# Performance work log

Hardware: AMD Instinct MI355X
Metric: run time of the kernel (lower is better)

The kernel has to match this reference:

```python
import jax, jax.numpy as jnp
import numpy as np
import math

B, H, S, D = 2, 12, 2048, 64

def setup_inputs() -> dict:
    key = jax.random.key(0)
    kq, kk, kv, km = jax.random.split(key, 4)
    Q = jax.random.normal(kq, (B, H, S, D), dtype=jnp.float32)
    K = jax.random.normal(kk, (B, H, S, D), dtype=jnp.float32)
    V = jax.random.normal(kv, (B, H, S, D), dtype=jnp.float32)
    mask = jax.random.randint(km, (B, 1, S, S), 0, 2, dtype=jnp.int32)
    return {"Q": Q, "K": K, "V": V, "mask": mask}

def reference(Q, K, V, mask):
    d_k = K.shape[-1]
    # [B,H,S,S] scores
    scores = jnp.einsum('bhqd,bhkd->bhqk', Q, K) / math.sqrt(d_k)
    scores = jnp.where(mask == 0, jnp.float32(-1e20), scores)
    attn = jax.nn.softmax(scores, axis=-1)
    # dropout p=0 -> identity
    return jnp.einsum('bhqk,bhkd->bhqd', attn, V)
```

## Files before the change

### kernel.cpp

```cpp
#include <hip/hip_runtime.h>
#include <hip/hip_bf16.h>
#include <math.h>


#define BB 2
#define HH 12
#define SS 2048
#define DD 64
#define BQ 128
#define BK 64
#define GG 2
#define KG (SS / GG)
#define NTG (KG / BK)
#define NQB (SS / BQ)
#define NBH (BB * HH)
#define LT 76
#define NROWS (BB * HH * SS)
#define QSCALE 0.1803368801111f

typedef __attribute__((ext_vector_type(8))) short bf8_t;
typedef __attribute__((ext_vector_type(4))) short bf4_t;
typedef __attribute__((ext_vector_type(4))) float f4_t;
typedef __attribute__((ext_vector_type(4))) unsigned u4_t;
typedef unsigned long long u64;

__device__ __forceinline__ short f2bf(float f) {
    __hip_bfloat16 h = __float2bfloat16(f);
    return *reinterpret_cast<short*>(&h);
}

__device__ __forceinline__ void gl_lds16(const void* g, void* l) {
    __builtin_amdgcn_global_load_lds(
        (const __attribute__((address_space(1))) unsigned*)(g),
        (__attribute__((address_space(3))) unsigned*)(l), 16, 0, 0);
}

__device__ __forceinline__ bf8_t ldfrag(const unsigned short* buf, int row, int c8) {
    return *(const bf8_t*)&buf[((row << 3) | (c8 ^ (row & 7))) << 3];
}

__global__ __launch_bounds__(256) void prepass(
    const float* __restrict__ V, const float* __restrict__ K,
    const int* __restrict__ M, unsigned short* __restrict__ Vt,
    unsigned short* __restrict__ Kb, u64* __restrict__ Mbt)
{
    __shared__ unsigned short Ts[64][LT];
    const int bx   = blockIdx.x;
    const int tid  = threadIdx.x;
    const int w    = tid >> 6;
    const int lane = tid & 63;
    const int b    = bx >> 11;
    const int row  = bx & 2047;

    {
        const int* src = M + (size_t)bx * SS;
        #pragma unroll
        for (int p = 0; p < 8; ++p) {
            int k = p * 256 + w * 64 + lane;
            u64 bm = __ballot(src[k] != 0);
            if (lane == 0)
                Mbt[(size_t)b * 32 * SS + (size_t)(p * 4 + w) * SS + row] = bm;
        }
    }

    if (bx < 768) {
        const int s0 = (bx & 31) * 64;
        const int bh = bx >> 5;
        const float* Vg = V + (size_t)bh * SS * DD;
        #pragma unroll
        for (int pass = 0; pass < 4; ++pass) {
            int c = tid + pass * 256;
            int r = c >> 4, col = (c & 15) * 4;
            float4 v = *(const float4*)(Vg + (size_t)(s0 + r) * DD + col);
            bf4_t p; p.x = f2bf(v.x); p.y = f2bf(v.y); p.z = f2bf(v.z); p.w = f2bf(v.w);
            *(bf4_t*)&Ts[r][col] = p;
        }
        __syncthreads();
        unsigned short* Vo = Vt + (size_t)bh * DD * SS;
        #pragma unroll
        for (int pass = 0; pass < 2; ++pass) {
            int c = tid + pass * 256;
            int d = c >> 3, sc = (c & 7) * 8;
            const int hh32 = sc & 32;
            const int qq4  = (sc >> 1) & 12;
            unsigned short t[8];
            #pragma unroll
            for (int u = 0; u < 4; ++u) t[u]     = Ts[hh32 + qq4 + u][d];
            #pragma unroll
            for (int u = 0; u < 4; ++u) t[4 + u] = Ts[hh32 + 16 + qq4 + u][d];
            uint4 o;
            o.x = (unsigned)t[0] | ((unsigned)t[1] << 16);
            o.y = (unsigned)t[2] | ((unsigned)t[3] << 16);
            o.z = (unsigned)t[4] | ((unsigned)t[5] << 16);
            o.w = (unsigned)t[6] | ((unsigned)t[7] << 16);
            *(uint4*)(Vo + (size_t)d * SS + s0 + sc) = o;
        }
    } else if (bx < 2304) {
        size_t i = ((size_t)(bx - 768) * 256 + tid) * 8;
        float4 a = *(const float4*)(K + i);
        float4 b2 = *(const float4*)(K + i + 4);
        uint4 o;
        o.x = (unsigned short)f2bf(a.x)  | ((unsigned)(unsigned short)f2bf(a.y)  << 16);
        o.y = (unsigned short)f2bf(a.z)  | ((unsigned)(unsigned short)f2bf(a.w)  << 16);
        o.z = (unsigned short)f2bf(b2.x) | ((unsigned)(unsigned short)f2bf(b2.y) << 16);
        o.w = (unsigned short)f2bf(b2.z) | ((unsigned)(unsigned short)f2bf(b2.w) << 16);
        *(uint4*)(Kb + i) = o;
    }
}

__global__ __launch_bounds__(256, 4) void attn_fwd(
    const float* __restrict__ Q, const unsigned short* __restrict__ Kb,
    const unsigned short* __restrict__ Vt, const u64* __restrict__ Mbt,
    float* __restrict__ Opart, float* __restrict__ Lpart)
{
    __shared__ unsigned short Ks[2 * BK * DD];
    __shared__ unsigned short Vts[2 * BK * DD];

    const int tid  = threadIdx.x;
    const int w    = tid >> 6;
    const int lane = tid & 63;
    const int quad = lane >> 4;
    const int l16  = lane & 15;
    const int bx   = blockIdx.x;
    const int qb   = bx / (NBH * GG);
    const int rem  = bx % (NBH * GG);
    const int g    = rem / NBH;
    const int bh   = rem % NBH;
    const int q0   = qb * BQ;
    const int b    = bh / HH;
    const int qbase = w * 32;

    const float*          Qg = Q  + (size_t)bh * SS * DD;
    const unsigned short* Kg = Kb + (size_t)bh * SS * DD;
    const unsigned short* Vg = Vt + (size_t)bh * DD * SS;
    float* Og = Opart + ((size_t)g * BB * HH + bh) * SS * DD;
    float* Lg = Lpart + (size_t)g * NROWS + (size_t)bh * SS;

    bf8_t bq[2][2];
    #pragma unroll
    for (int qf = 0; qf < 2; ++qf)
        #pragma unroll
        for (int ks = 0; ks < 2; ++ks) {
            const float* qp = Qg + (size_t)(q0 + qbase + qf * 16 + l16) * DD
                                 + ks * 32 + quad * 8;
            float4 x = *(const float4*)qp;
            float4 y = *(const float4*)(qp + 4);
            bf8_t f;
            f[0] = f2bf(x.x * QSCALE); f[1] = f2bf(x.y * QSCALE);
            f[2] = f2bf(x.z * QSCALE); f[3] = f2bf(x.w * QSCALE);
            f[4] = f2bf(y.x * QSCALE); f[5] = f2bf(y.y * QSCALE);
            f[6] = f2bf(y.z * QSCALE); f[7] = f2bf(y.w * QSCALE);
            bq[qf][ks] = f;
        }

    bf8_t onesf;
    {
        short ov = (l16 == 0) ? (short)0x3F80 : (short)0;
        #pragma unroll
        for (int j = 0; j < 8; ++j) onesf[j] = ov;
    }

    f4_t oacc[2][4], lacc[2];
    #pragma unroll
    for (int qf = 0; qf < 2; ++qf) {
        lacc[qf] = (f4_t){0.f, 0.f, 0.f, 0.f};
        #pragma unroll
        for (int nf = 0; nf < 4; ++nf) oacc[qf][nf] = (f4_t){0.f, 0.f, 0.f, 0.f};
    }

    const unsigned short* kSrc[2];
    const unsigned short* vSrc[2];
    unsigned short*       kDst[2];
    unsigned short*       vDst[2];
    #pragma unroll
    for (int j = 0; j < 2; ++j) {
        const int bc = (w * 2 + j) * 64;
        const int c  = bc + lane;
        const int r  = c >> 3;
        const int c8 = (c & 7) ^ (r & 7);
        kSrc[j] = Kg + (size_t)(g * KG + r) * DD + c8 * 8;
        vSrc[j] = Vg + (size_t)r * SS + g * KG + c8 * 8;
        kDst[j] = Ks  + bc * 8;
        vDst[j] = Vts + bc * 8;
    }
    const u64* mp[2];
    u64 mpf[2];
    #pragma unroll
    for (int qf = 0; qf < 2; ++qf) {
        mp[qf] = Mbt + (size_t)b * 32 * SS + (size_t)(g * NTG) * SS
                     + q0 + qbase + qf * 16 + l16;
        mpf[qf] = *mp[qf];
    }

    #pragma unroll
    for (int j = 0; j < 2; ++j) {
        gl_lds16(kSrc[j], kDst[j]);
        gl_lds16(vSrc[j], vDst[j]);
        kSrc[j] += BK * DD;
        vSrc[j] += BK;
    }
    __syncthreads();

    for (int t = 0; t < NTG; ++t) {
        const int cb = (t & 1) * (BK * DD);
        if (t + 1 < NTG) {
            const int nb = ((t + 1) & 1) * (BK * DD);
            #pragma unroll
            for (int j = 0; j < 2; ++j) {
                gl_lds16(kSrc[j], kDst[j] + nb);
                gl_lds16(vSrc[j], vDst[j] + nb);
                kSrc[j] += BK * DD;
                vSrc[j] += BK;
            }
        }
        const u64 cm[2] = {mpf[0] >> (quad * 4), mpf[1] >> (quad * 4)};
        if (t + 1 < NTG) {
            #pragma unroll
            for (int qf = 0; qf < 2; ++qf) {
                mp[qf] += SS;
                mpf[qf] = *mp[qf];
            }
        }
        const unsigned short* Kst = Ks  + cb;
        const unsigned short* Vst = Vts + cb;

        #pragma unroll
        for (int h = 0; h < 2; ++h) {
            unsigned aw[2][4];
            #pragma unroll
            for (int kfh = 0; kfh < 2; ++kfh) {
                const int kf = h * 2 + kfh;
                bf8_t ak0 = ldfrag(Kst, kf * 16 + l16, quad);
                bf8_t ak1 = ldfrag(Kst, kf * 16 + l16, 4 + quad);
                #pragma unroll
                for (int qf = 0; qf < 2; ++qf) {
                    f4_t s = (f4_t){0.f, 0.f, 0.f, 0.f};
                    s = __builtin_amdgcn_mfma_f32_16x16x32_bf16(ak0, bq[qf][0], s, 0, 0, 0);
                    s = __builtin_amdgcn_mfma_f32_16x16x32_bf16(ak1, bq[qf][1], s, 0, 0, 0);
                    float e[4];
                    #pragma unroll
                    for (int r = 0; r < 4; ++r) {
                        float v = __builtin_amdgcn_exp2f(s[r]);
                        e[r] = ((cm[qf] >> (kf * 16 + r)) & 1ull) ? v : 0.f;
                    }
                    aw[qf][kfh * 2 + 0] = __builtin_amdgcn_perm(
                        __float_as_uint(e[1]), __float_as_uint(e[0]), 0x07060302u);
                    aw[qf][kfh * 2 + 1] = __builtin_amdgcn_perm(
                        __float_as_uint(e[3]), __float_as_uint(e[2]), 0x07060302u);
                }
            }
            bf8_t ap[2];
            __builtin_amdgcn_s_setprio(1);
            #pragma unroll
            for (int qf = 0; qf < 2; ++qf) {
                u4_t wds = (u4_t){aw[qf][0], aw[qf][1], aw[qf][2], aw[qf][3]};
                ap[qf] = __builtin_bit_cast(bf8_t, wds);
                lacc[qf] = __builtin_amdgcn_mfma_f32_16x16x32_bf16(
                    ap[qf], onesf, lacc[qf], 0, 0, 0);
            }
            #pragma unroll
            for (int nf = 0; nf < 4; ++nf) {
                bf8_t bv = ldfrag(Vst, nf * 16 + l16, h * 4 + quad);
                #pragma unroll
                for (int qf = 0; qf < 2; ++qf)
                    oacc[qf][nf] = __builtin_amdgcn_mfma_f32_16x16x32_bf16(
                        ap[qf], bv, oacc[qf][nf], 0, 0, 0);
            }
            __builtin_amdgcn_s_setprio(0);
        }
        if (t + 1 < NTG) __syncthreads();
    }

    #pragma unroll
    for (int qf = 0; qf < 2; ++qf) {
        #pragma unroll
        for (int r = 0; r < 4; ++r) {
            const int row = q0 + qbase + qf * 16 + quad * 4 + r;
            #pragma unroll
            for (int nf = 0; nf < 4; ++nf)
                Og[(size_t)row * DD + nf * 16 + l16] = oacc[qf][nf][r];
        }
        if (l16 == 0) {
            #pragma unroll
            for (int r = 0; r < 4; ++r)
                Lg[q0 + qbase + qf * 16 + quad * 4 + r] = lacc[qf][r];
        }
    }
}

__global__ __launch_bounds__(256) void reduce_o(
    const float* __restrict__ Opart, const float* __restrict__ Lpart,
    float* __restrict__ O)
{
    const size_t idx = (size_t)blockIdx.x * 256 + threadIdx.x;
    const size_t row = idx >> 4;
    const int    c   = (int)(idx & 15) * 4;
    float4 acc = {0.f, 0.f, 0.f, 0.f};
    float  l   = 0.f;
    #pragma unroll
    for (int g = 0; g < GG; ++g) {
        float4 a = *(const float4*)(Opart + ((size_t)g * NROWS + row) * DD + c);
        acc.x += a.x; acc.y += a.y; acc.z += a.z; acc.w += a.w;
        l += Lpart[(size_t)g * NROWS + row];
    }
    const float inv = 1.f / l;
    float4 o;
    o.x = acc.x * inv; o.y = acc.y * inv; o.z = acc.z * inv; o.w = acc.w * inv;
    *(float4*)(O + row * DD + c) = o;
}

extern "C" void kernel_launch(void* const* d_in, const int* in_sizes, int n_in,
                              void* d_out, int out_size, void* d_ws, size_t ws_size,
                              hipStream_t stream) {
    const float* Q = (const float*)d_in[0];
    const float* K = (const float*)d_in[1];
    const float* V = (const float*)d_in[2];
    const int*   M = (const int*)d_in[3];
    float*       O = (float*)d_out;

    unsigned short* Vt    = (unsigned short*)d_ws;
    unsigned short* Kb    = Vt + (size_t)BB * HH * SS * DD;
    u64*            Mbt   = (u64*)(Kb + (size_t)BB * HH * SS * DD);
    float*          Opart = (float*)(Mbt + (size_t)BB * 32 * SS);
    float*          Lpart = Opart + (size_t)GG * NROWS * DD;

    prepass<<<dim3(BB * SS), 256, 0, stream>>>(V, K, M, Vt, Kb, Mbt);
    attn_fwd<<<dim3(NQB * NBH * GG), 256, 0, stream>>>(Q, Kb, Vt, Mbt,
                                                       Opart, Lpart);
    reduce_o<<<dim3((NROWS * DD / 4) / 256), 256, 0, stream>>>(Opart, Lpart, O);
}
```

Measured before the change: 149.5 us.

## Load K and V MFMA fragments directly from global memory, dropping LDS staging

Removes the double-buffered LDS staging of K and V tiles (global_load_lds plus block barriers). Each wave now reads its MFMA operand fragments straight from global memory through per-lane pointers. This eliminates LDS traffic and __syncthreads, but the four waves of a block each fetch the same K/V data separately and global latency is no longer hidden by prefetch, so the kernel leans on L1/L2 hits.

```diff
diff --git a/kernel.cpp b/kernel.cpp
--- a/kernel.cpp
+++ b/kernel.cpp
@@ -29,16 +29,6 @@
     return *reinterpret_cast<short*>(&h);
 }
 
-__device__ __forceinline__ void gl_lds16(const void* g, void* l) {
-    __builtin_amdgcn_global_load_lds(
-        (const __attribute__((address_space(1))) unsigned*)(g),
-        (__attribute__((address_space(3))) unsigned*)(l), 16, 0, 0);
-}
-
-__device__ __forceinline__ bf8_t ldfrag(const unsigned short* buf, int row, int c8) {
-    return *(const bf8_t*)&buf[((row << 3) | (c8 ^ (row & 7))) << 3];
-}
-
 __global__ __launch_bounds__(256) void prepass(
     const float* __restrict__ V, const float* __restrict__ K,
     const int* __restrict__ M, unsigned short* __restrict__ Vt,
@@ -113,9 +103,6 @@
     const unsigned short* __restrict__ Vt, const u64* __restrict__ Mbt,
     float* __restrict__ Opart, float* __restrict__ Lpart)
 {
-    __shared__ unsigned short Ks[2 * BK * DD];
-    __shared__ unsigned short Vts[2 * BK * DD];
-
     const int tid  = threadIdx.x;
     const int w    = tid >> 6;
     const int lane = tid & 63;
@@ -168,21 +155,15 @@
         for (int nf = 0; nf < 4; ++nf) oacc[qf][nf] = (f4_t){0.f, 0.f, 0.f, 0.f};
     }
 
-    const unsigned short* kSrc[2];
-    const unsigned short* vSrc[2];
-    unsigned short*       kDst[2];
-    unsigned short*       vDst[2];
-    #pragma unroll
-    for (int j = 0; j < 2; ++j) {
-        const int bc = (w * 2 + j) * 64;
-        const int c  = bc + lane;
-        const int r  = c >> 3;
-        const int c8 = (c & 7) ^ (r & 7);
-        kSrc[j] = Kg + (size_t)(g * KG + r) * DD + c8 * 8;
-        vSrc[j] = Vg + (size_t)r * SS + g * KG + c8 * 8;
-        kDst[j] = Ks  + bc * 8;
-        vDst[j] = Vts + bc * 8;
-    }
+    const unsigned short* kp[4];
+    #pragma unroll
+    for (int kf = 0; kf < 4; ++kf)
+        kp[kf] = Kg + (size_t)(g * KG + kf * 16 + l16) * DD + quad * 8;
+    const unsigned short* vp[4];
+    #pragma unroll
+    for (int nf = 0; nf < 4; ++nf)
+        vp[nf] = Vg + (size_t)(nf * 16 + l16) * SS + g * KG + quad * 8;
+
     const u64* mp[2];
     u64 mpf[2];
     #pragma unroll
@@ -192,27 +173,7 @@
         mpf[qf] = *mp[qf];
     }
 
-    #pragma unroll
-    for (int j = 0; j < 2; ++j) {
-        gl_lds16(kSrc[j], kDst[j]);
-        gl_lds16(vSrc[j], vDst[j]);
-        kSrc[j] += BK * DD;
-        vSrc[j] += BK;
-    }
-    __syncthreads();
-
     for (int t = 0; t < NTG; ++t) {
-        const int cb = (t & 1) * (BK * DD);
-        if (t + 1 < NTG) {
-            const int nb = ((t + 1) & 1) * (BK * DD);
-            #pragma unroll
-            for (int j = 0; j < 2; ++j) {
-                gl_lds16(kSrc[j], kDst[j] + nb);
-                gl_lds16(vSrc[j], vDst[j] + nb);
-                kSrc[j] += BK * DD;
-                vSrc[j] += BK;
-            }
-        }
         const u64 cm[2] = {mpf[0] >> (quad * 4), mpf[1] >> (quad * 4)};
         if (t + 1 < NTG) {
             #pragma unroll
@@ -221,8 +182,6 @@
                 mpf[qf] = *mp[qf];
             }
         }
-        const unsigned short* Kst = Ks  + cb;
-        const unsigned short* Vst = Vts + cb;
 
         #pragma unroll
         for (int h = 0; h < 2; ++h) {
@@ -230,8 +189,8 @@
             #pragma unroll
             for (int kfh = 0; kfh < 2; ++kfh) {
                 const int kf = h * 2 + kfh;
-                bf8_t ak0 = ldfrag(Kst, kf * 16 + l16, quad);
-                bf8_t ak1 = ldfrag(Kst, kf * 16 + l16, 4 + quad);
+                bf8_t ak0 = *(const bf8_t*)(kp[kf]);
+                bf8_t ak1 = *(const bf8_t*)(kp[kf] + 32);
                 #pragma unroll
                 for (int qf = 0; qf < 2; ++qf) {
                     f4_t s = (f4_t){0.f, 0.f, 0.f, 0.f};
@@ -260,7 +219,7 @@
             }
             #pragma unroll
             for (int nf = 0; nf < 4; ++nf) {
-                bf8_t bv = ldfrag(Vst, nf * 16 + l16, h * 4 + quad);
+                bf8_t bv = *(const bf8_t*)(vp[nf] + h * 32);
                 #pragma unroll
                 for (int qf = 0; qf < 2; ++qf)
                     oacc[qf][nf] = __builtin_amdgcn_mfma_f32_16x16x32_bf16(
@@ -268,7 +227,10 @@
             }
             __builtin_amdgcn_s_setprio(0);
         }
-        if (t + 1 < NTG) __syncthreads();
+        #pragma unroll
+        for (int kf = 0; kf < 4; ++kf) kp[kf] += BK * DD;
+        #pragma unroll
+        for (int nf = 0; nf < 4; ++nf) vp[nf] += BK;
     }
 
     #pragma unroll
```

New measurement: 205.7 us. +37.6%, slower.
